# Kernel optimization log

Measured on AMD Instinct MI355X. Metric: run time of the kernel, lower is better.

The kernel has to match this reference:

```python
import jax, jax.numpy as jnp
import numpy as np
import math

E = 2048         # n_embd
H = 16           # num query head pairs (num_heads)
HKV = 8          # num_kv_heads
NREP = H // HKV  # 2
HD = E // H // 2 # head_dim = 64
DEPTH = 12
LAMBDA_INIT = 0.8 - 0.6 * math.exp(-0.3 * DEPTH)
EPS = 1e-6


def setup_inputs() -> dict:
    key = jax.random.key(0)
    ks = jax.random.split(key, 10)
    s = lambda fan_in: 1.0 / np.sqrt(fan_in)
    return {
        "x": jax.random.normal(ks[0], (2, 2048, E), jnp.float32),
        "Wq": jax.random.normal(ks[1], (E, E), jnp.float32) * s(E),
        "Wk": jax.random.normal(ks[2], (E, E // NREP), jnp.float32) * s(E),
        "Wv": jax.random.normal(ks[3], (E, E // NREP), jnp.float32) * s(E),
        "Wo": jax.random.normal(ks[4], (E, E), jnp.float32) * s(E),
        "lam_q1": jax.random.normal(ks[5], (HD,), jnp.float32) * 0.1,
        "lam_k1": jax.random.normal(ks[6], (HD,), jnp.float32) * 0.1,
        "lam_q2": jax.random.normal(ks[7], (HD,), jnp.float32) * 0.1,
        "lam_k2": jax.random.normal(ks[8], (HD,), jnp.float32) * 0.1,
        "g": jnp.ones((2 * HD,), jnp.float32),  # RMSNorm weight
    }


def _rotary(x, cos, sin):
    # x: [B, T, nh, HD]; cos/sin: [T, HD//2]
    d = x.shape[-1] // 2
    x1, x2 = x[..., :d], x[..., d:]
    c = cos[None, :, None, :]
    si = sin[None, :, None, :]
    return jnp.concatenate([x1 * c + x2 * si, -x1 * si + x2 * c], axis=-1)


def reference(x, Wq, Wk, Wv, Wo, lam_q1, lam_k1, lam_q2, lam_k2, g):
    B, T, _ = x.shape
    q = (x @ Wq).reshape(B, T, 2 * H, HD)
    k = (x @ Wk).reshape(B, T, 2 * HKV, HD)
    v = (x @ Wv).reshape(B, T, HKV, 2 * HD)

    inv_freq = 1.0 / (10000.0 ** (jnp.arange(0, HD, 2, dtype=jnp.float32) / HD))
    freqs = jnp.arange(T, dtype=jnp.float32)[:, None] * inv_freq[None, :]
    cos, sin = jnp.cos(freqs), jnp.sin(freqs)
    q = _rotary(q, cos, sin)
    k = _rotary(k, cos, sin)

    q = jnp.transpose(q, (0, 2, 1, 3)) * (HD ** -0.5)   # [B, 2H, T, HD]
    k = jnp.repeat(jnp.transpose(k, (0, 2, 1, 3)), NREP, axis=1)  # [B, 2H, T, HD]
    v = jnp.repeat(jnp.transpose(v, (0, 2, 1, 3)), NREP, axis=1)  # [B, H, T, 2HD]

    scores = jnp.einsum('bhtd,bhsd->bhts', q, k)
    scores = jnp.nan_to_num(scores)
    mask = jnp.triu(jnp.full((T, T), -jnp.inf, scores.dtype), 1)
    scores = scores + mask
    p = jax.nn.softmax(scores.astype(jnp.float32), axis=-1).astype(scores.dtype)

    lam1 = jnp.exp(jnp.sum(lam_q1 * lam_k1))
    lam2 = jnp.exp(jnp.sum(lam_q2 * lam_k2))
    lam = lam1 - lam2 + LAMBDA_INIT

    p = p.reshape(B, H, 2, T, T)
    diff = p[:, :, 0] - lam * p[:, :, 1]               # [B, H, T, T]
    attn = jnp.einsum('bhts,bhsd->bhtd', diff, v)      # [B, H, T, 2HD]

    # RMSNorm over last dim (2*HD)
    attn = attn * jax.lax.rsqrt(jnp.mean(attn * attn, axis=-1, keepdims=True) + EPS) * g
    attn = attn * (1.0 - LAMBDA_INIT)
    attn = jnp.transpose(attn, (0, 2, 1, 3)).reshape(B, T, E)
    return attn @ Wo
```

## Files before the change

### kernel.cpp

```cpp
#include <hip/hip_runtime.h>

#define T_SEQ 2048

typedef __bf16 bf16x8 __attribute__((ext_vector_type(8)));
typedef float f32x4 __attribute__((ext_vector_type(4)));
typedef unsigned short u16;

__device__ __forceinline__ u16 f2b(float f) {
  unsigned u = __float_as_uint(f);
  unsigned r = 0x7fffu + ((u >> 16) & 1u);
  return (u16)((u + r) >> 16);
}
__device__ __forceinline__ float b2f(u16 v) {
  return __uint_as_float(((unsigned)v) << 16);
}
__device__ __forceinline__ f32x4 mfma16(bf16x8 a, bf16x8 b, f32x4 c) {
  return __builtin_amdgcn_mfma_f32_16x16x32_bf16(a, b, c, 0, 0, 0);
}
__device__ __forceinline__ unsigned pkhi(float lo, float hi) {
  return __builtin_amdgcn_perm(__float_as_uint(hi), __float_as_uint(lo), 0x07060302u);
}
__device__ __forceinline__ void glds16(const void* g, void* s) {
  __builtin_amdgcn_global_load_lds(
      (const __attribute__((address_space(1))) void*)(uintptr_t)g,
      (__attribute__((address_space(3))) void*)(unsigned)(uintptr_t)s, 16, 0, 0);
}

__global__ void lam_kernel(const float* __restrict__ q1, const float* __restrict__ k1,
                           const float* __restrict__ q2, const float* __restrict__ k2,
                           float* __restrict__ outp) {
  int l = threadIdx.x;
  float a = q1[l] * k1[l];
  float c = q2[l] * k2[l];
  #pragma unroll
  for (int off = 32; off > 0; off >>= 1) {
    a += __shfl_down(a, off);
    c += __shfl_down(c, off);
  }
  if (l == 0) outp[0] = expf(a) - expf(c) + 0.7836057665316244f;
}

__global__ __launch_bounds__(256) void convert_kernel(const float* __restrict__ in,
                                                      u16* __restrict__ outp, int n) {
  int i = (blockIdx.x * 256 + threadIdx.x) * 4;
  if (i >= n) return;
  float4 v = *(const float4*)(in + i);
  ushort4 pk;
  pk.x = f2b(v.x); pk.y = f2b(v.y); pk.z = f2b(v.z); pk.w = f2b(v.w);
  *(ushort4*)(outp + i) = pk;
}

__global__ __launch_bounds__(256) void transpose_kernel(const float* __restrict__ in,
                                                        u16* __restrict__ outp, int R, int C) {
  __shared__ float tile[32][33];
  int c0 = blockIdx.x * 32, r0 = blockIdx.y * 32;
  int tx = threadIdx.x & 31, ty = threadIdx.x >> 5;
  #pragma unroll
  for (int k2 = 0; k2 < 4; k2++)
    tile[ty * 4 + k2][tx] = in[(size_t)(r0 + ty * 4 + k2) * C + c0 + tx];
  __syncthreads();
  #pragma unroll
  for (int k2 = 0; k2 < 4; k2++)
    outp[(size_t)(c0 + ty * 4 + k2) * R + r0 + tx] = f2b(tile[tx][ty * 4 + k2]);
}

template <bool OUT_BF16>
__global__ __launch_bounds__(256) void gemm128_kernel(const u16* __restrict__ A,
                                                      const u16* __restrict__ BT,
                                                      void* __restrict__ C, int N, int K) {
  __shared__ alignas(16) u16 As[128 * 64];
  __shared__ alignas(16) u16 Bs[128 * 64];
  const int tid = threadIdx.x, w = tid >> 6, lane = tid & 63;
  const int l15 = lane & 15, quad = lane >> 4;
  const int m0 = blockIdx.y * 128, n0 = blockIdx.x * 128;
  const int wm = (w >> 1) * 64, wn = (w & 1) * 64;
  const int lr = lane >> 3, slot = lane & 7, csw = slot ^ lr;
  f32x4 acc[4][4];
  #pragma unroll
  for (int mt = 0; mt < 4; mt++)
    #pragma unroll
    for (int nt = 0; nt < 4; nt++) acc[mt][nt] = (f32x4){0.f, 0.f, 0.f, 0.f};
  const u16* Ag = A + (size_t)(m0 + w * 32 + lr) * K + csw * 8;
  const u16* Bg = BT + (size_t)(n0 + w * 32 + lr) * K + csw * 8;
  u16* Asd = As + (w * 32) * 64;
  u16* Bsd = Bs + (w * 32) * 64;
  for (int kt = 0; kt < K; kt += 64) {
    #pragma unroll
    for (int i = 0; i < 4; i++) {
      glds16(Ag + kt + (size_t)(i * 8) * K, Asd + i * 512);
      glds16(Bg + kt + (size_t)(i * 8) * K, Bsd + i * 512);
    }
    __syncthreads();
    #pragma unroll
    for (int kk = 0; kk < 2; kk++) {
      bf16x8 am[4], bn[4];
      #pragma unroll
      for (int t = 0; t < 4; t++) {
        const int ra = wm + t * 16 + l15;
        am[t] = *(const bf16x8*)&As[ra * 64 + (((kk * 4 + quad) ^ (ra & 7)) << 3)];
        const int rb = wn + t * 16 + l15;
        bn[t] = *(const bf16x8*)&Bs[rb * 64 + (((kk * 4 + quad) ^ (rb & 7)) << 3)];
      }
      #pragma unroll
      for (int mt = 0; mt < 4; mt++)
        #pragma unroll
        for (int nt = 0; nt < 4; nt++) acc[mt][nt] = mfma16(am[mt], bn[nt], acc[mt][nt]);
    }
    __syncthreads();
  }
  const int row = m0 + wm + quad * 4;
  #pragma unroll
  for (int mt = 0; mt < 4; mt++) {
    #pragma unroll
    for (int nt = 0; nt < 4; nt++) {
      const int col = n0 + wn + nt * 16 + l15;
      #pragma unroll
      for (int rr = 0; rr < 4; rr++) {
        if (OUT_BF16)
          ((u16*)C)[(size_t)(row + mt * 16 + rr) * N + col] = f2b(acc[mt][nt][rr]);
        else
          ((float*)C)[(size_t)(row + mt * 16 + rr) * N + col] = acc[mt][nt][rr];
      }
    }
  }
}

__global__ __launch_bounds__(256) void rotary_kernel(const u16* __restrict__ qkv,
                                                     u16* __restrict__ outp, int lh,
                                                     int colbase, float scale) {
  int idx = blockIdx.x * 256 + threadIdx.x;
  int i = idx & 31;
  int h = (idx >> 5) & ((1 << lh) - 1);
  int bt = idx >> (5 + lh);
  int t = bt & (T_SEQ - 1);
  size_t inb = (size_t)bt * 4096 + colbase + h * 64 + i;
  float x1 = b2f(qkv[inb]);
  float x2 = b2f(qkv[inb + 32]);
  float invf = exp2f(-(float)i * 0.4152410118609203f);
  float ang = (float)t * invf;
  float c = cosf(ang), s = sinf(ang);
  float o1 = (x1 * c + x2 * s) * scale;
  float o2 = (x2 * c - x1 * s) * scale;
  size_t ob = ((size_t)((bt >> 11) * (1 << lh) + h) * T_SEQ + t) * 64 + i;
  outp[ob] = f2b(o1);
  outp[ob + 32] = f2b(o2);
}

__global__ __launch_bounds__(256) void vtrans_kernel(const u16* __restrict__ qkv,
                                                     u16* __restrict__ outp) {
  __shared__ unsigned tile[32][33];
  int bh = blockIdx.z;
  int t0 = blockIdx.x * 32, dv0 = blockIdx.y * 32;
  int tx = threadIdx.x & 31, ty = threadIdx.x >> 5;
  int bt_base = (bh >> 3) * T_SEQ;
  int col = 3072 + (bh & 7) * 128 + dv0 + tx;
  #pragma unroll
  for (int k2 = 0; k2 < 4; k2++)
    tile[ty * 4 + k2][tx] = qkv[(size_t)(bt_base + t0 + ty * 4 + k2) * 4096 + col];
  __syncthreads();
  #pragma unroll
  for (int k2 = 0; k2 < 4; k2++)
    outp[((size_t)bh * 128 + dv0 + ty * 4 + k2) * T_SEQ + t0 + tx] = (u16)tile[tx][ty * 4 + k2];
}

__global__ __launch_bounds__(256) void attn_kernel(const u16* __restrict__ Qb,
                                                   const u16* __restrict__ Kb,
                                                   const u16* __restrict__ Vt,
                                                   const float* __restrict__ lamp,
                                                   const float* __restrict__ g,
                                                   u16* __restrict__ attn_out) {
  __shared__ alignas(16) u16 Ks[64 * 64];
  __shared__ alignas(16) u16 Vs[128 * 64];
  __shared__ alignas(16) u16 Ps[4][16][136];
  const int pr = blockIdx.x;
  const int bh = blockIdx.y;
  const int b = bh >> 4, h = bh & 15;
  const int tid = threadIdx.x, w = tid >> 6, lane = tid & 63;
  const int l15 = lane & 15, quad = lane >> 4;
  const int lr = lane >> 3, slot = lane & 7, csw = slot ^ lr;
  const float lam = lamp[0];

  const u16* Kbase = Kb + (size_t)(b * 16 + h) * T_SEQ * 64;
  const u16* Vbase = Vt + (size_t)(b * 8 + (h >> 1)) * 128 * T_SEQ;
  const u16* Kg = Kbase + (size_t)(w * 16 + lr) * 64 + csw * 8;
  const u16* Vg = Vbase + (size_t)(w * 32 + lr) * T_SEQ + csw * 8;

  #pragma unroll 1
  for (int half = 0; half < 2; half++) {
    const int tt = half ? 31 - pr : pr;
    const int qb = tt * 64 + w * 16;
    const int qglob = qb + l15;

    bf16x8 qf[2][2];
    #pragma unroll
    for (int e = 0; e < 2; e++)
      #pragma unroll
      for (int kk = 0; kk < 2; kk++)
        qf[e][kk] = *(const bf16x8*)&Qb[((size_t)(b * 32 + 2 * h + e) * T_SEQ + qb + l15) * 64 +
                                        kk * 32 + quad * 8];

    f32x4 o[2][8];
    float lsum[2] = {0.f, 0.f};
    #pragma unroll
    for (int e = 0; e < 2; e++)
      #pragma unroll
      for (int nt = 0; nt < 8; nt++) o[e][nt] = (f32x4){0.f, 0.f, 0.f, 0.f};

    for (int st = 0; st <= tt; st++) {
      const int s0 = st * 64;
      glds16(Kg + (size_t)s0 * 64, &Ks[(w * 16) * 64]);
      glds16(Kg + (size_t)(s0 + 8) * 64, &Ks[(w * 16 + 8) * 64]);
      #pragma unroll
      for (int i = 0; i < 4; i++)
        glds16(Vg + s0 + (size_t)(i * 8) * T_SEQ, &Vs[(w * 32 + i * 8) * 64]);
      __syncthreads();

      bf16x8 kf[4][2];
      #pragma unroll
      for (int j = 0; j < 4; j++) {
        const int rk = j * 16 + l15;
        #pragma unroll
        for (int kk = 0; kk < 2; kk++)
          kf[j][kk] = *(const bf16x8*)&Ks[rk * 64 + (((kk * 4 + quad) ^ (rk & 7)) << 3)];
      }

      #pragma unroll
      for (int e = 0; e < 2; e++) {
        f32x4 sc[4];
        #pragma unroll
        for (int j = 0; j < 4; j++) {
          f32x4 z = {0.f, 0.f, 0.f, 0.f};
          z = mfma16(kf[j][0], qf[e][0], z);
          sc[j] = mfma16(kf[j][1], qf[e][1], z);
        }
        if (st == tt) {
          #pragma unroll
          for (int j = 0; j < 4; j++) {
            int srow = s0 + j * 16 + quad * 4;
            #pragma unroll
            for (int rr = 0; rr < 4; rr++)
              if (srow + rr > qglob) sc[j][rr] = -1e30f;
          }
        }
        float ls = 0.f;
        #pragma unroll
        for (int j = 0; j < 4; j++) {
          #pragma unroll
          for (int rr = 0; rr < 4; rr++) {
            float p = exp2f(sc[j][rr]);
            sc[j][rr] = p;
            ls += p;
          }
          uint2 pk;
          pk.x = pkhi(sc[j][0], sc[j][1]);
          pk.y = pkhi(sc[j][2], sc[j][3]);
          *(uint2*)&Ps[w][l15][e * 64 + j * 16 + quad * 4] = pk;
        }
        lsum[e] += ls;
      }
      asm volatile("s_waitcnt lgkmcnt(0)" ::: "memory");
      bf16x8 pa[2][2];
      #pragma unroll
      for (int e = 0; e < 2; e++)
        #pragma unroll
        for (int kk = 0; kk < 2; kk++)
          pa[e][kk] = *(const bf16x8*)&Ps[w][l15][e * 64 + kk * 32 + quad * 8];
      asm volatile("" ::: "memory");
      #pragma unroll
      for (int nt = 0; nt < 8; nt++) {
        const int rv = nt * 16 + l15;
        bf16x8 vf0 = *(const bf16x8*)&Vs[rv * 64 + ((quad ^ (rv & 7)) << 3)];
        bf16x8 vf1 = *(const bf16x8*)&Vs[rv * 64 + (((4 + quad) ^ (rv & 7)) << 3)];
        o[0][nt] = mfma16(vf0, pa[0][0], o[0][nt]);
        o[0][nt] = mfma16(vf1, pa[0][1], o[0][nt]);
        o[1][nt] = mfma16(vf0, pa[1][0], o[1][nt]);
        o[1][nt] = mfma16(vf1, pa[1][1], o[1][nt]);
      }
      __syncthreads();
    }

    float l0 = lsum[0], l1 = lsum[1];
    l0 += __shfl_xor(l0, 16); l0 += __shfl_xor(l0, 32);
    l1 += __shfl_xor(l1, 16); l1 += __shfl_xor(l1, 32);
    const float il0 = 1.f / l0, il1 = lam / l1;
    float ssq = 0.f;
    #pragma unroll
    for (int nt = 0; nt < 8; nt++)
      #pragma unroll
      for (int rr = 0; rr < 4; rr++) {
        float v = o[0][nt][rr] * il0 - o[1][nt][rr] * il1;
        o[0][nt][rr] = v;
        ssq += v * v;
      }
    ssq += __shfl_xor(ssq, 16);
    ssq += __shfl_xor(ssq, 32);
    const float rsc = rsqrtf(ssq * (1.f / 128.f) + 1e-6f) * 0.2163942334683756f;
    #pragma unroll
    for (int nt = 0; nt < 8; nt++) {
      float4 gv = *(const float4*)&g[nt * 16 + quad * 4];
      uint2 pk;
      pk.x = (unsigned)f2b(o[0][nt][0] * rsc * gv.x) |
             ((unsigned)f2b(o[0][nt][1] * rsc * gv.y) << 16);
      pk.y = (unsigned)f2b(o[0][nt][2] * rsc * gv.z) |
             ((unsigned)f2b(o[0][nt][3] * rsc * gv.w) << 16);
      *(uint2*)&Ps[w][l15][nt * 16 + quad * 4] = pk;
    }
    asm volatile("s_waitcnt lgkmcnt(0)" ::: "memory");
    #pragma unroll
    for (int i = 0; i < 4; i++) {
      const int r = (lane >> 4) + i * 4, c = (lane & 15) * 8;
      bf16x8 ov = *(const bf16x8*)&Ps[w][r][c];
      *(bf16x8*)&attn_out[(size_t)(b * T_SEQ + qb + r) * 2048 + h * 128 + c] = ov;
    }
    __syncthreads();
  }
}

extern "C" void kernel_launch(void* const* d_in, const int* in_sizes, int n_in, void* d_out,
                              int out_size, void* d_ws, size_t ws_size, hipStream_t stream) {
  const float* x = (const float*)d_in[0];
  const float* Wq = (const float*)d_in[1];
  const float* Wk = (const float*)d_in[2];
  const float* Wv = (const float*)d_in[3];
  const float* Wo = (const float*)d_in[4];
  const float* lq1 = (const float*)d_in[5];
  const float* lk1 = (const float*)d_in[6];
  const float* lq2 = (const float*)d_in[7];
  const float* lk2 = (const float*)d_in[8];
  const float* g = (const float*)d_in[9];

  char* ws = (char*)d_ws;
  u16* WT = (u16*)(ws);
  u16* WoT = (u16*)(ws + 16777216);
  u16* xbf = (u16*)(ws + 25165824);
  u16* QKV = (u16*)(ws + 41943040);
  u16* Qb = (u16*)(ws + 75497472);
  u16* Kb = (u16*)(ws + 92274688);
  u16* Vt = (u16*)(ws + 100663296);
  u16* Attn = (u16*)(ws + 109051904);
  float* lam = (float*)(ws + 125829120);

  lam_kernel<<<1, 64, 0, stream>>>(lq1, lk1, lq2, lk2, lam);
  convert_kernel<<<8192, 256, 0, stream>>>(x, xbf, 8388608);
  transpose_kernel<<<dim3(64, 64), 256, 0, stream>>>(Wq, WT, 2048, 2048);
  transpose_kernel<<<dim3(32, 64), 256, 0, stream>>>(Wk, WT + (size_t)2048 * 2048, 2048, 1024);
  transpose_kernel<<<dim3(32, 64), 256, 0, stream>>>(Wv, WT + (size_t)3072 * 2048, 2048, 1024);
  transpose_kernel<<<dim3(64, 64), 256, 0, stream>>>(Wo, WoT, 2048, 2048);
  gemm128_kernel<true><<<dim3(32, 32), 256, 0, stream>>>(xbf, WT, QKV, 4096, 2048);
  rotary_kernel<<<16384, 256, 0, stream>>>(QKV, Qb, 5, 0, 0.18033688011112042f);
  rotary_kernel<<<8192, 256, 0, stream>>>(QKV, Kb, 4, 2048, 1.0f);
  vtrans_kernel<<<dim3(64, 4, 16), 256, 0, stream>>>(QKV, Vt);
  attn_kernel<<<dim3(16, 32), 256, 0, stream>>>(Qb, Kb, Vt, lam, g, Attn);
  gemm128_kernel<false><<<dim3(16, 32), 256, 0, stream>>>(Attn, WoT, d_out, 2048, 2048);
}
```

Measured before the change: 386.0 us.

## Merge weight transposes and rotary launches, tile V layout, use raw exp2

Folds the four weight-transpose launches into a single kernel writing one contiguous transposed buffer, and merges the Q and K rotary launches into one. V is stored tiled in 64-position blocks so each attention tile loads from a contiguous region. The softmax exponent now calls the hardware v_exp_f32 instead of the library exp2f. Together these cut launch overhead and simplify attention address arithmetic, though the raw exp skips the range handling that exp2f provides.

Measured after the change: 368.7 us. -4.5%, faster.

```diff
diff --git a/kernel.cpp b/kernel.cpp
--- a/kernel.cpp
+++ b/kernel.cpp
@@ -19,6 +19,20 @@
 }
 __device__ __forceinline__ unsigned pkhi(float lo, float hi) {
   return __builtin_amdgcn_perm(__float_as_uint(hi), __float_as_uint(lo), 0x07060302u);
+}
+#if defined(__has_builtin)
+#if __has_builtin(__builtin_amdgcn_exp2f)
+#define HAVE_RAW_EXP2 1
+#endif
+#endif
+__device__ __forceinline__ float exp2r(float x) {
+#ifdef HAVE_RAW_EXP2
+  return __builtin_amdgcn_exp2f(x);
+#else
+  float r;
+  asm("v_exp_f32 %0, %1" : "=v"(r) : "v"(x));
+  return r;
+#endif
 }
 __device__ __forceinline__ void glds16(const void* g, void* s) {
   __builtin_amdgcn_global_load_lds(
@@ -50,18 +64,28 @@
   *(ushort4*)(outp + i) = pk;
 }
 
-__global__ __launch_bounds__(256) void transpose_kernel(const float* __restrict__ in,
-                                                        u16* __restrict__ outp, int R, int C) {
+__global__ __launch_bounds__(256) void transposeW_kernel(const float* __restrict__ Wq,
+                                                         const float* __restrict__ Wk,
+                                                         const float* __restrict__ Wv,
+                                                         const float* __restrict__ Wo,
+                                                         u16* __restrict__ outp) {
   __shared__ float tile[32][33];
-  int c0 = blockIdx.x * 32, r0 = blockIdx.y * 32;
-  int tx = threadIdx.x & 31, ty = threadIdx.x >> 5;
+  const int ro0 = blockIdx.y * 32;
+  const int r0 = blockIdx.x * 32;
+  const float* src; int C, cbase;
+  if (ro0 < 2048)      { src = Wq; C = 2048; cbase = 0; }
+  else if (ro0 < 3072) { src = Wk; C = 1024; cbase = 2048; }
+  else if (ro0 < 4096) { src = Wv; C = 1024; cbase = 3072; }
+  else                 { src = Wo; C = 2048; cbase = 4096; }
+  const int cs0 = ro0 - cbase;
+  const int tx = threadIdx.x & 31, ty = threadIdx.x >> 5;
   #pragma unroll
   for (int k2 = 0; k2 < 4; k2++)
-    tile[ty * 4 + k2][tx] = in[(size_t)(r0 + ty * 4 + k2) * C + c0 + tx];
+    tile[ty * 4 + k2][tx] = src[(size_t)(r0 + ty * 4 + k2) * C + cs0 + tx];
   __syncthreads();
   #pragma unroll
   for (int k2 = 0; k2 < 4; k2++)
-    outp[(size_t)(c0 + ty * 4 + k2) * R + r0 + tx] = f2b(tile[tx][ty * 4 + k2]);
+    outp[(size_t)(ro0 + ty * 4 + k2) * 2048 + r0 + tx] = f2b(tile[tx][ty * 4 + k2]);
 }
 
 template <bool OUT_BF16>
@@ -126,22 +150,27 @@
 }
 
 __global__ __launch_bounds__(256) void rotary_kernel(const u16* __restrict__ qkv,
-                                                     u16* __restrict__ outp, int lh,
-                                                     int colbase, float scale) {
+                                                     u16* __restrict__ Qb,
+                                                     u16* __restrict__ Kb, float qscale) {
   int idx = blockIdx.x * 256 + threadIdx.x;
   int i = idx & 31;
-  int h = (idx >> 5) & ((1 << lh) - 1);
-  int bt = idx >> (5 + lh);
-  int t = bt & (T_SEQ - 1);
-  size_t inb = (size_t)bt * 4096 + colbase + h * 64 + i;
+  int bt = (idx >> 5) & 4095;
+  int hh = idx >> 17;
+  int t = bt & (T_SEQ - 1), b = bt >> 11;
+  bool isq = hh < 32;
+  int col = isq ? hh * 64 : 2048 + (hh - 32) * 64;
+  size_t inb = (size_t)bt * 4096 + col + i;
   float x1 = b2f(qkv[inb]);
   float x2 = b2f(qkv[inb + 32]);
   float invf = exp2f(-(float)i * 0.4152410118609203f);
   float ang = (float)t * invf;
   float c = cosf(ang), s = sinf(ang);
+  float scale = isq ? qscale : 1.0f;
   float o1 = (x1 * c + x2 * s) * scale;
   float o2 = (x2 * c - x1 * s) * scale;
-  size_t ob = ((size_t)((bt >> 11) * (1 << lh) + h) * T_SEQ + t) * 64 + i;
+  u16* outp = isq ? (Qb + (size_t)(b * 32 + hh) * (T_SEQ * 64))
+                  : (Kb + (size_t)(b * 16 + hh - 32) * (T_SEQ * 64));
+  size_t ob = (size_t)t * 64 + i;
   outp[ob] = f2b(o1);
   outp[ob + 32] = f2b(o2);
 }
@@ -158,9 +187,12 @@
   for (int k2 = 0; k2 < 4; k2++)
     tile[ty * 4 + k2][tx] = qkv[(size_t)(bt_base + t0 + ty * 4 + k2) * 4096 + col];
   __syncthreads();
-  #pragma unroll
-  for (int k2 = 0; k2 < 4; k2++)
-    outp[((size_t)bh * 128 + dv0 + ty * 4 + k2) * T_SEQ + t0 + tx] = (u16)tile[tx][ty * 4 + k2];
+  const int stile = t0 >> 6, sin = (t0 & 63) + tx;
+  #pragma unroll
+  for (int k2 = 0; k2 < 4; k2++) {
+    int dv = dv0 + ty * 4 + k2;
+    outp[(((size_t)bh * 32 + stile) * 128 + dv) * 64 + sin] = (u16)tile[tx][ty * 4 + k2];
+  }
 }
 
 __global__ __launch_bounds__(256) void attn_kernel(const u16* __restrict__ Qb,
@@ -180,10 +212,10 @@
   const int lr = lane >> 3, slot = lane & 7, csw = slot ^ lr;
   const float lam = lamp[0];
 
-  const u16* Kbase = Kb + (size_t)(b * 16 + h) * T_SEQ * 64;
-  const u16* Vbase = Vt + (size_t)(b * 8 + (h >> 1)) * 128 * T_SEQ;
-  const u16* Kg = Kbase + (size_t)(w * 16 + lr) * 64 + csw * 8;
-  const u16* Vg = Vbase + (size_t)(w * 32 + lr) * T_SEQ + csw * 8;
+  const u16* Kg = Kb + (size_t)(b * 16 + h) * (T_SEQ * 64) + (w * 16 + lr) * 64 + csw * 8;
+  const u16* Vg = Vt + (size_t)(b * 8 + (h >> 1)) * (T_SEQ * 128) + w * 2048 + lr * 64 + csw * 8;
+  u16* kd = &Ks[w * 1024];
+  u16* vd = &Vs[w * 2048];
 
   #pragma unroll 1
   for (int half = 0; half < 2; half++) {
@@ -207,12 +239,11 @@
       for (int nt = 0; nt < 8; nt++) o[e][nt] = (f32x4){0.f, 0.f, 0.f, 0.f};
 
     for (int st = 0; st <= tt; st++) {
-      const int s0 = st * 64;
-      glds16(Kg + (size_t)s0 * 64, &Ks[(w * 16) * 64]);
-      glds16(Kg + (size_t)(s0 + 8) * 64, &Ks[(w * 16 + 8) * 64]);
-      #pragma unroll
-      for (int i = 0; i < 4; i++)
-        glds16(Vg + s0 + (size_t)(i * 8) * T_SEQ, &Vs[(w * 32 + i * 8) * 64]);
+      const u16* kp = Kg + st * 4096;
+      const u16* vp = Vg + st * 8192;
+      glds16(kp, kd); glds16(kp + 512, kd + 512);
+      glds16(vp, vd); glds16(vp + 512, vd + 512);
+      glds16(vp + 1024, vd + 1024); glds16(vp + 1536, vd + 1536);
       __syncthreads();
 
       bf16x8 kf[4][2];
@@ -236,7 +267,7 @@
         if (st == tt) {
           #pragma unroll
           for (int j = 0; j < 4; j++) {
-            int srow = s0 + j * 16 + quad * 4;
+            int srow = st * 64 + j * 16 + quad * 4;
             #pragma unroll
             for (int rr = 0; rr < 4; rr++)
               if (srow + rr > qglob) sc[j][rr] = -1e30f;
@@ -247,7 +278,7 @@
         for (int j = 0; j < 4; j++) {
           #pragma unroll
           for (int rr = 0; rr < 4; rr++) {
-            float p = exp2f(sc[j][rr]);
+            float p = exp2r(sc[j][rr]);
             sc[j][rr] = p;
             ls += p;
           }
@@ -331,7 +362,6 @@
 
   char* ws = (char*)d_ws;
   u16* WT = (u16*)(ws);
-  u16* WoT = (u16*)(ws + 16777216);
   u16* xbf = (u16*)(ws + 25165824);
   u16* QKV = (u16*)(ws + 41943040);
   u16* Qb = (u16*)(ws + 75497472);
@@ -342,14 +372,11 @@
 
   lam_kernel<<<1, 64, 0, stream>>>(lq1, lk1, lq2, lk2, lam);
   convert_kernel<<<8192, 256, 0, stream>>>(x, xbf, 8388608);
-  transpose_kernel<<<dim3(64, 64), 256, 0, stream>>>(Wq, WT, 2048, 2048);
-  transpose_kernel<<<dim3(32, 64), 256, 0, stream>>>(Wk, WT + (size_t)2048 * 2048, 2048, 1024);
-  transpose_kernel<<<dim3(32, 64), 256, 0, stream>>>(Wv, WT + (size_t)3072 * 2048, 2048, 1024);
-  transpose_kernel<<<dim3(64, 64), 256, 0, stream>>>(Wo, WoT, 2048, 2048);
+  transposeW_kernel<<<dim3(64, 192), 256, 0, stream>>>(Wq, Wk, Wv, Wo, WT);
   gemm128_kernel<true><<<dim3(32, 32), 256, 0, stream>>>(xbf, WT, QKV, 4096, 2048);
-  rotary_kernel<<<16384, 256, 0, stream>>>(QKV, Qb, 5, 0, 0.18033688011112042f);
-  rotary_kernel<<<8192, 256, 0, stream>>>(QKV, Kb, 4, 2048, 1.0f);
+  rotary_kernel<<<24576, 256, 0, stream>>>(QKV, Qb, Kb, 0.18033688011112042f);
   vtrans_kernel<<<dim3(64, 4, 16), 256, 0, stream>>>(QKV, Vt);
   attn_kernel<<<dim3(16, 32), 256, 0, stream>>>(Qb, Kb, Vt, lam, g, Attn);
-  gemm128_kernel<false><<<dim3(16, 32), 256, 0, stream>>>(Attn, WoT, d_out, 2048, 2048);
-}
+  gemm128_kernel<false><<<dim3(16, 32), 256, 0, stream>>>(Attn, WT + (size_t)4096 * 2048, d_out,
+                                                          2048, 2048);
+}
```
